# Optimization experiments

Measured on AMD Instinct MI355X. Metric: run time of the kernel, lower is better.

## Reference

```python
import jax, jax.numpy as jnp
import numpy as np

N_NODES = 100000
N_EDGES = 1600000
D_FEAT = 64


def setup_inputs() -> dict:
    key = jax.random.key(0)
    k1, k2, k3, k4 = jax.random.split(key, 4)
    rows = jax.random.randint(k1, (N_EDGES,), 0, N_NODES, dtype=jnp.int32)
    cols = jax.random.randint(k2, (N_EDGES,), 0, N_NODES, dtype=jnp.int32)
    # nonnegative edge weights, like a normalized adjacency
    vals = jax.random.uniform(k3, (N_EDGES,), dtype=jnp.float32)
    embeds = jax.random.normal(k4, (N_NODES, D_FEAT), dtype=jnp.float32)
    return {"rows": rows, "cols": cols, "vals": vals, "embeds": embeds}


def reference(rows, cols, vals, embeds):
    # SpMM: out[r] = sum_{e: rows[e]==r} vals[e] * embeds[cols[e]]
    gathered = embeds[cols] * vals[:, None]        # [E, d]
    out = jax.ops.segment_sum(gathered, rows, num_segments=embeds.shape[0])  # [N, d]
    return out
```

## Files before the change

kernel.cpp:

```cpp
#include <hip/hip_runtime.h>

#define D_FEAT 64
#define NN 100000
#define SBROWS 512
#define NSB ((NN + SBROWS - 1) / SBROWS)
#define CAP 10240
#define BATCH 4096
#define OFFP (SBROWS + 1)

__global__ void __launch_bounds__(256) quant_prep(const float* __restrict__ embeds,
                                                  char* __restrict__ e8,
                                                  float* __restrict__ scales,
                                                  int* __restrict__ ccursors) {
    if (blockIdx.x == 0 && threadIdx.x < NSB) ccursors[threadIdx.x] = threadIdx.x * CAP;
    int w = threadIdx.x >> 6, lane = threadIdx.x & 63;
    int nwaves = gridDim.x * 4;
    for (int row = blockIdx.x * 4 + w; row < NN; row += nwaves) {
        float f = embeds[((size_t)row << 6) + lane];
        float a = fabsf(f);
        #pragma unroll
        for (int off = 32; off > 0; off >>= 1) a = fmaxf(a, __shfl_xor(a, off));
        float inv = (a > 0.f) ? 127.0f / a : 0.f;
        int q = __float2int_rn(f * inv);
        e8[((size_t)row << 6) + lane] = (char)q;
        if (lane == 0) scales[row] = a * (1.0f / 127.0f);
    }
}

__global__ void __launch_bounds__(512) coarse_split(const int* __restrict__ rows,
                                                    const int* __restrict__ cols,
                                                    const float* __restrict__ vals,
                                                    const float* __restrict__ scales,
                                                    int* __restrict__ ccursors,
                                                    int2* __restrict__ tmp, int E) {
    __shared__ int2 pay[BATCH];
    __shared__ int hist[NSB], scanv[NSB], lcur[NSB], gbase[NSB], wlim[NSB];
    __shared__ int tsum[256];

    int b0 = blockIdx.x * BATCH;
    int n = E - b0; if (n > BATCH) n = BATCH;
    int t = threadIdx.x;

    for (int i = t; i < NSB; i += 512) hist[i] = 0;
    __syncthreads();

    for (int k = t; k < n; k += 512)
        atomicAdd(&hist[rows[b0 + k] >> 9], 1);
    __syncthreads();

    if (t < 256) tsum[t] = (t < NSB) ? hist[t] : 0;
    __syncthreads();
    for (int off = 1; off < 256; off <<= 1) {
        int x = 0;
        if (t < 256 && t >= off) x = tsum[t - off];
        __syncthreads();
        if (t < 256) tsum[t] += x;
        __syncthreads();
    }
    if (t < NSB) {
        int excl = (t > 0) ? tsum[t - 1] : 0;
        scanv[t] = excl;
        lcur[t]  = excl;
        int cnt = hist[t];
        int gb  = atomicAdd(&ccursors[t], cnt);
        int lim = t * CAP + CAP;
        int wl  = lim - gb; if (wl < 0) wl = 0; if (wl > cnt) wl = cnt;
        gbase[t] = gb; wlim[t] = wl;
    }
    __syncthreads();

    for (int k = t; k < n; k += 512) {
        int r  = rows[b0 + k];
        int c  = cols[b0 + k];
        float vv = vals[b0 + k] * scales[c];
        int sb = r >> 9;
        int idx = atomicAdd(&lcur[sb], 1);
        pay[idx] = make_int2(c | ((r & 511) << 17), __float_as_int(vv));
    }
    __syncthreads();

    int wv = t >> 6, ln = t & 63;
    for (int s = wv; s < NSB; s += 8) {
        int sv = scanv[s], gb = gbase[s], wl = wlim[s];
        for (int j = ln; j < wl; j += 64) tmp[gb + j] = pay[sv + j];
    }
}

__global__ void __launch_bounds__(1024) fine_split(const int2* __restrict__ tmp,
                                                   const int* __restrict__ ccursors,
                                                   int* __restrict__ offsets,
                                                   int2* __restrict__ sedges) {
    __shared__ int lhist[SBROWS], lbase[SBROWS], lcur[SBROWS], tt[SBROWS];
    int sb = blockIdx.x;
    int t = threadIdx.x;
    int cstart = sb * CAP;
    int cnt = ccursors[sb] - cstart; if (cnt > CAP) cnt = CAP;
    int cend = cstart + cnt;

    if (t < SBROWS) lhist[t] = 0;
    __syncthreads();

    for (int i = cstart + t; i < cend; i += 1024)
        atomicAdd(&lhist[(tmp[i].x >> 17) & 511], 1);
    __syncthreads();

    if (t < SBROWS) tt[t] = lhist[t];
    __syncthreads();
    for (int off = 1; off < SBROWS; off <<= 1) {
        int x = 0;
        if (t < SBROWS && t >= off) x = tt[t - off];
        __syncthreads();
        if (t < SBROWS) tt[t] += x;
        __syncthreads();
    }
    if (t < SBROWS) {
        int excl = (t > 0) ? tt[t - 1] : 0;
        lbase[t] = cstart + excl;
        lcur[t]  = 0;
        offsets[sb * OFFP + t] = cstart + excl;
    }
    if (t == 0) offsets[sb * OFFP + SBROWS] = cend;
    __syncthreads();

    for (int i = cstart + t; i < cend; i += 1024) {
        int2 p = tmp[i];
        int fl = (p.x >> 17) & 511;
        int pos = lbase[fl] + atomicAdd(&lcur[fl], 1);
        sedges[pos] = make_int2(p.x & 0x1FFFF, p.y);
    }
}

__global__ void __launch_bounds__(256) row_spmm(const int* __restrict__ offsets,
                                                const int2* __restrict__ sedges,
                                                const char* __restrict__ e8,
                                                float* __restrict__ out) {
    __shared__ int2 stage[4][64];
    int w    = threadIdx.x >> 6;
    int lane = threadIdx.x & 63;
    int r0   = (blockIdx.x * 4 + w) * 4;
    int sb   = r0 >> 9;
    int obase = sb * OFFP + (r0 & 511);

    #pragma unroll
    for (int k = 0; k < 4; k++) {
        int row = r0 + k;
        int s = offsets[obase + k], e = offsets[obase + k + 1];
        float acc = 0.f;
        for (int base = s; base < e; base += 64) {
            int idx = base + lane;
            int2 se = (idx < e) ? sedges[idx] : make_int2(0, 0);
            stage[w][lane] = se;
            int m = e - base; if (m > 64) m = 64;
            int nsub = (m + 15) >> 4;
            for (int sub = 0; sub < nsub; sub++) {
                #pragma unroll
                for (int jj = 0; jj < 16; jj++) {
                    int2  sv = stage[w][sub * 16 + jj];
                    float vs = __int_as_float(sv.y);
                    float g  = (float)e8[(sv.x << 6) + lane];
                    acc = fmaf(vs, g, acc);
                }
            }
        }
        out[((size_t)row << 6) + lane] = acc;
    }
}

__global__ void spmm_atomic_kernel(const int* __restrict__ rows, const int* __restrict__ cols,
                                   const float* __restrict__ vals, const float* __restrict__ embeds,
                                   float* __restrict__ out, int n_edges) {
    long long t = (long long)blockIdx.x * blockDim.x + threadIdx.x;
    int e = (int)(t >> 4);
    int f4 = ((int)t & 15) * 4;
    if (e >= n_edges) return;
    int r = rows[e], c = cols[e];
    float v = vals[e];
    const float4 emb = *reinterpret_cast<const float4*>(&embeds[(long long)c * D_FEAT + f4]);
    float* o = &out[(long long)r * D_FEAT + f4];
    atomicAdd(o + 0, v * emb.x);
    atomicAdd(o + 1, v * emb.y);
    atomicAdd(o + 2, v * emb.z);
    atomicAdd(o + 3, v * emb.w);
}

extern "C" void kernel_launch(void* const* d_in, const int* in_sizes, int n_in,
                              void* d_out, int out_size, void* d_ws, size_t ws_size,
                              hipStream_t stream) {
    const int*   rows   = (const int*)d_in[0];
    const int*   cols   = (const int*)d_in[1];
    const float* vals   = (const float*)d_in[2];
    const float* embeds = (const float*)d_in[3];
    float*       out    = (float*)d_out;
    int E = in_sizes[0];

    size_t need = (size_t)NSB * CAP * 16 + (size_t)NN * D_FEAT
                + (size_t)NN * 4 + ((size_t)NSB * OFFP + NSB) * 4;

    if (ws_size >= need && E <= NSB * CAP) {
        char* ws = (char*)d_ws;
        int2*   tmp     = (int2*)ws;        ws += (size_t)NSB * CAP * 8;
        int2*   sedges  = (int2*)ws;        ws += (size_t)NSB * CAP * 8;
        char*   e8      = (char*)ws;        ws += (size_t)NN * D_FEAT;
        float*  scales  = (float*)ws;       ws += (size_t)NN * 4;
        int*    offsets = (int*)ws;         ws += (size_t)NSB * OFFP * 4;
        int*    ccursors= (int*)ws;

        quant_prep<<<2048, 256, 0, stream>>>(embeds, e8, scales, ccursors);

        int nb1 = (E + BATCH - 1) / BATCH;
        coarse_split<<<nb1, 512, 0, stream>>>(rows, cols, vals, scales, ccursors, tmp, E);
        fine_split<<<NSB, 1024, 0, stream>>>(tmp, ccursors, offsets, sedges);

        row_spmm<<<NN / 16, 256, 0, stream>>>(offsets, sedges, e8, out);
    } else {
        hipMemsetAsync(d_out, 0, (size_t)out_size * sizeof(float), stream);
        long long total = (long long)E * 16;
        int block = 256;
        spmm_atomic_kernel<<<(int)((total + block - 1) / block), block, 0, stream>>>(
            rows, cols, vals, embeds, out, E);
    }
}
```

Before: 92.50 us.

## Fuse embedding quantization into coarse split kernel and defer scale multiply

Merges the int8 quantization pass into the coarse bucketing kernel by appending extra blocks that quantize embeddings, so the two independent phases run concurrently in one launch. The per-edge scale multiply moves from coarse_split to fine_split, which breaks the dependency on scales being ready before bucketing. Cursor initialization becomes a memset with relative offsets. It saves one launch and overlaps the memory-bound quantization with the edge scatter, but quantize blocks scheduled late may become a tail.

```diff
diff --git a/kernel.cpp b/kernel.cpp
--- a/kernel.cpp
+++ b/kernel.cpp
@@ -7,35 +7,37 @@
 #define CAP 10240
 #define BATCH 4096
 #define OFFP (SBROWS + 1)
-
-__global__ void __launch_bounds__(256) quant_prep(const float* __restrict__ embeds,
-                                                  char* __restrict__ e8,
-                                                  float* __restrict__ scales,
-                                                  int* __restrict__ ccursors) {
-    if (blockIdx.x == 0 && threadIdx.x < NSB) ccursors[threadIdx.x] = threadIdx.x * CAP;
-    int w = threadIdx.x >> 6, lane = threadIdx.x & 63;
-    int nwaves = gridDim.x * 4;
-    for (int row = blockIdx.x * 4 + w; row < NN; row += nwaves) {
-        float f = embeds[((size_t)row << 6) + lane];
-        float a = fabsf(f);
-        #pragma unroll
-        for (int off = 32; off > 0; off >>= 1) a = fmaxf(a, __shfl_xor(a, off));
-        float inv = (a > 0.f) ? 127.0f / a : 0.f;
-        int q = __float2int_rn(f * inv);
-        e8[((size_t)row << 6) + lane] = (char)q;
-        if (lane == 0) scales[row] = a * (1.0f / 127.0f);
-    }
-}
-
-__global__ void __launch_bounds__(512) coarse_split(const int* __restrict__ rows,
-                                                    const int* __restrict__ cols,
-                                                    const float* __restrict__ vals,
-                                                    const float* __restrict__ scales,
-                                                    int* __restrict__ ccursors,
-                                                    int2* __restrict__ tmp, int E) {
+#define NCONV 128
+
+__global__ void __launch_bounds__(512) fused_split_quant(const int* __restrict__ rows,
+                                                         const int* __restrict__ cols,
+                                                         const float* __restrict__ vals,
+                                                         const float* __restrict__ embeds,
+                                                         char* __restrict__ e8,
+                                                         float* __restrict__ scales,
+                                                         int* __restrict__ ccursors,
+                                                         int2* __restrict__ tmp,
+                                                         int E, int nb1) {
     __shared__ int2 pay[BATCH];
     __shared__ int hist[NSB], scanv[NSB], lcur[NSB], gbase[NSB], wlim[NSB];
     __shared__ int tsum[256];
+
+    if (blockIdx.x >= nb1) {
+        int cb = blockIdx.x - nb1;
+        int w = threadIdx.x >> 6, lane = threadIdx.x & 63;
+        int nw = NCONV * 8;
+        for (int row = cb * 8 + w; row < NN; row += nw) {
+            float f = embeds[((size_t)row << 6) + lane];
+            float a = fabsf(f);
+            #pragma unroll
+            for (int off = 32; off > 0; off >>= 1) a = fmaxf(a, __shfl_xor(a, off));
+            float inv = (a > 0.f) ? 127.0f / a : 0.f;
+            int q = __float2int_rn(f * inv);
+            e8[((size_t)row << 6) + lane] = (char)q;
+            if (lane == 0) scales[row] = a * (1.0f / 127.0f);
+        }
+        return;
+    }
 
     int b0 = blockIdx.x * BATCH;
     int n = E - b0; if (n > BATCH) n = BATCH;
@@ -62,20 +64,18 @@
         scanv[t] = excl;
         lcur[t]  = excl;
         int cnt = hist[t];
-        int gb  = atomicAdd(&ccursors[t], cnt);
-        int lim = t * CAP + CAP;
-        int wl  = lim - gb; if (wl < 0) wl = 0; if (wl > cnt) wl = cnt;
-        gbase[t] = gb; wlim[t] = wl;
+        int old = atomicAdd(&ccursors[t], cnt);
+        int wl  = CAP - old; if (wl < 0) wl = 0; if (wl > cnt) wl = cnt;
+        gbase[t] = t * CAP + old;
+        wlim[t]  = wl;
     }
     __syncthreads();
 
     for (int k = t; k < n; k += 512) {
         int r  = rows[b0 + k];
-        int c  = cols[b0 + k];
-        float vv = vals[b0 + k] * scales[c];
         int sb = r >> 9;
         int idx = atomicAdd(&lcur[sb], 1);
-        pay[idx] = make_int2(c | ((r & 511) << 17), __float_as_int(vv));
+        pay[idx] = make_int2(cols[b0 + k] | ((r & 511) << 17), __float_as_int(vals[b0 + k]));
     }
     __syncthreads();
 
@@ -88,13 +88,14 @@
 
 __global__ void __launch_bounds__(1024) fine_split(const int2* __restrict__ tmp,
                                                    const int* __restrict__ ccursors,
+                                                   const float* __restrict__ scales,
                                                    int* __restrict__ offsets,
                                                    int2* __restrict__ sedges) {
     __shared__ int lhist[SBROWS], lbase[SBROWS], lcur[SBROWS], tt[SBROWS];
     int sb = blockIdx.x;
     int t = threadIdx.x;
     int cstart = sb * CAP;
-    int cnt = ccursors[sb] - cstart; if (cnt > CAP) cnt = CAP;
+    int cnt = ccursors[sb]; if (cnt > CAP) cnt = CAP;
     int cend = cstart + cnt;
 
     if (t < SBROWS) lhist[t] = 0;
@@ -124,9 +125,11 @@
 
     for (int i = cstart + t; i < cend; i += 1024) {
         int2 p = tmp[i];
+        int c  = p.x & 0x1FFFF;
+        float vv = __int_as_float(p.y) * scales[c];
         int fl = (p.x >> 17) & 511;
         int pos = lbase[fl] + atomicAdd(&lcur[fl], 1);
-        sedges[pos] = make_int2(p.x & 0x1FFFF, p.y);
+        sedges[pos] = make_int2(c, __float_as_int(vv));
     }
 }
 
@@ -205,11 +208,12 @@
         int*    offsets = (int*)ws;         ws += (size_t)NSB * OFFP * 4;
         int*    ccursors= (int*)ws;
 
-        quant_prep<<<2048, 256, 0, stream>>>(embeds, e8, scales, ccursors);
+        hipMemsetAsync(ccursors, 0, (size_t)NSB * 4, stream);
 
         int nb1 = (E + BATCH - 1) / BATCH;
-        coarse_split<<<nb1, 512, 0, stream>>>(rows, cols, vals, scales, ccursors, tmp, E);
-        fine_split<<<NSB, 1024, 0, stream>>>(tmp, ccursors, offsets, sedges);
+        fused_split_quant<<<nb1 + NCONV, 512, 0, stream>>>(rows, cols, vals, embeds,
+                                                           e8, scales, ccursors, tmp, E, nb1);
+        fine_split<<<NSB, 1024, 0, stream>>>(tmp, ccursors, scales, offsets, sedges);
 
         row_spmm<<<NN / 16, 256, 0, stream>>>(offsets, sedges, e8, out);
     } else {
```

Measured after the change: 128.7 us. 1.39x slower.
